# Optimization experiments

Measured on AMD Instinct MI355X. Metric: run time of the kernel, lower is better.

## Reference

```python
import jax, jax.numpy as jnp
import numpy as np

D_MODEL = 1024
NUM_HEADS = 16
D_K = D_MODEL // NUM_HEADS


def setup_inputs() -> dict:
    key = jax.random.key(0)
    kx, kq, kk, kv, ko = jax.random.split(key, 5)
    B, S = 4, 2048
    scale = 1.0 / np.sqrt(D_MODEL)
    return {
        "x": jax.random.normal(kx, (B, S, D_MODEL), dtype=jnp.float32),
        "W_q": jax.random.normal(kq, (D_MODEL, D_MODEL), dtype=jnp.float32) * scale,
        "W_k": jax.random.normal(kk, (D_MODEL, D_MODEL), dtype=jnp.float32) * scale,
        "W_v": jax.random.normal(kv, (D_MODEL, D_MODEL), dtype=jnp.float32) * scale,
        "W_o": jax.random.normal(ko, (D_MODEL, D_MODEL), dtype=jnp.float32) * scale,
    }


def reference(x, W_q, W_k, W_v, W_o):
    B, S, _ = x.shape
    # torch Linear: y = x @ W.T
    def proj(W):
        return (x @ W.T).reshape(B, S, NUM_HEADS, D_K).transpose(0, 2, 1, 3)  # [B,H,S,Dk]
    Q, K, V = proj(W_q), proj(W_k), proj(W_v)
    scores = jnp.einsum("bhqd,bhkd->bhqk", Q, K) / jnp.sqrt(jnp.float32(D_K))
    attn = jax.nn.softmax(scores, axis=-1)
    out = jnp.einsum("bhqk,bhkd->bhqd", attn, V)  # [B,H,S,Dk]
    out = out.transpose(0, 2, 1, 3).reshape(B, S, D_MODEL)
    return out @ W_o.T
```

## Files before the change

### kernel.cpp

```cpp
#include <hip/hip_runtime.h>
#include <hip/hip_bf16.h>

typedef unsigned short u16;
typedef __bf16 bf16x8 __attribute__((ext_vector_type(8)));
typedef float f32x4 __attribute__((ext_vector_type(4)));

#define DEV static __device__ __forceinline__

DEV u16 f2b(float f){
  union { float f; unsigned u; } v; v.f = f;
  unsigned r = (v.u + 0x7FFFu + ((v.u >> 16) & 1u)) >> 16;
  return (u16)r;
}

DEV unsigned pack2(float lo, float hi){
  __hip_bfloat162 h = __float22bfloat162_rn(float2{lo, hi});
  union { __hip_bfloat162 h; unsigned u; } c; c.h = h;
  return c.u;
}

DEV unsigned pack_trunc(float lo, float hi){
  union { float f; unsigned u; } a, b; a.f = lo; b.f = hi;
  return __builtin_amdgcn_perm(b.u, a.u, 0x07060302u);
}

DEV void gload16(const void* g, void* l){
  __builtin_amdgcn_global_load_lds((const __attribute__((address_space(1))) void*)g,
                                   (__attribute__((address_space(3))) void*)l, 16, 0, 0);
}

DEV f32x4 mfma16(bf16x8 a, bf16x8 b, f32x4 c){
  return __builtin_amdgcn_mfma_f32_16x16x32_bf16(a, b, c, 0, 0, 0);
}

__global__ void cvt_kernel(const float* __restrict__ src, u16* __restrict__ dst, int n4){
  int i = blockIdx.x * 256 + threadIdx.x;
  if (i < n4){
    float4 v = reinterpret_cast<const float4*>(src)[i];
    ushort4 o;
    o.x = f2b(v.x); o.y = f2b(v.y); o.z = f2b(v.z); o.w = f2b(v.w);
    reinterpret_cast<ushort4*>(dst)[i] = o;
  }
}

template<int MODE>
__global__ __launch_bounds__(256, 2)
void gemm_nt(const u16* __restrict__ A, const u16* __restrict__ B, void* __restrict__ Out, float scale){
  __shared__ __align__(16) u16 lsA[128*64];
  __shared__ __align__(16) u16 lsB[128*64];
  const int tid  = threadIdx.x;
  const int lane = tid & 63, wid = tid >> 6;
  const int g = lane >> 4, c15 = lane & 15;
  const int m0 = blockIdx.x * 128, n0 = blockIdx.y * 128;
  const int wm = (wid >> 1) * 64, wn = (wid & 1) * 64;
  const f32x4 vzero = {0.f, 0.f, 0.f, 0.f};

  f32x4 acc[4][4];
#pragma unroll
  for (int mi = 0; mi < 4; ++mi)
#pragma unroll
    for (int ni = 0; ni < 4; ++ni) acc[mi][ni] = vzero;

  for (int kt = 0; kt < 16; ++kt){
    __syncthreads();
#pragma unroll
    for (int i = 0; i < 4; ++i){
      int c = i * 256 + tid;
      int row = c >> 3, gc = (c & 7) ^ (row & 7);
      const u16* src;
      if constexpr (MODE == 2){
        int b = m0 >> 11, s = (m0 & 2047) + row;
        src = A + (((size_t)(b * 16 + kt) * 2048 + s) << 6) + (gc << 3);
      } else {
        src = A + ((size_t)(m0 + row) << 10) + (kt << 6) + (gc << 3);
      }
      gload16(src, lsA + (size_t)c * 8);
    }
#pragma unroll
    for (int i = 0; i < 4; ++i){
      int c = i * 256 + tid;
      int row = c >> 3, gc = (c & 7) ^ (row & 7);
      const u16* src = B + ((size_t)(n0 + row) << 10) + (kt << 6) + (gc << 3);
      gload16(src, lsB + (size_t)c * 8);
    }
    __syncthreads();

    bf16x8 af[4][2], bf[4][2];
#pragma unroll
    for (int mi = 0; mi < 4; ++mi)
#pragma unroll
      for (int kk = 0; kk < 2; ++kk){
        int ra = wm + mi * 16 + c15;
        af[mi][kk] = *reinterpret_cast<const bf16x8*>(lsA + ra * 64 + ((((kk << 2) + g) ^ (ra & 7)) << 3));
        int rb = wn + mi * 16 + c15;
        bf[mi][kk] = *reinterpret_cast<const bf16x8*>(lsB + rb * 64 + ((((kk << 2) + g) ^ (rb & 7)) << 3));
      }
#pragma unroll
    for (int mi = 0; mi < 4; ++mi)
#pragma unroll
      for (int ni = 0; ni < 4; ++ni){
        acc[mi][ni] = mfma16(af[mi][0], bf[ni][0], acc[mi][ni]);
        acc[mi][ni] = mfma16(af[mi][1], bf[ni][1], acc[mi][ni]);
      }
  }

#pragma unroll
  for (int mi = 0; mi < 4; ++mi)
#pragma unroll
    for (int ni = 0; ni < 4; ++ni){
      int mrow = m0 + wm + mi * 16 + g * 4;
      int ncol = n0 + wn + ni * 16 + c15;
      if constexpr (MODE == 0){
        int b = mrow >> 11, s = mrow & 2047;
        int h = ncol >> 6, dk = ncol & 63;
        u16* dst = (u16*)Out + (((size_t)(b * 16 + h) * 2048 + s) << 6) + dk;
#pragma unroll
        for (int r = 0; r < 4; ++r) dst[(size_t)r << 6] = f2b(acc[mi][ni][r] * scale);
      } else if constexpr (MODE == 1){
        int b = mrow >> 11, s = mrow & 2047;
        int h = ncol >> 6, dk = ncol & 63;
        ushort4 o;
        o.x = f2b(acc[mi][ni][0]); o.y = f2b(acc[mi][ni][1]);
        o.z = f2b(acc[mi][ni][2]); o.w = f2b(acc[mi][ni][3]);
        *reinterpret_cast<ushort4*>((u16*)Out + (((size_t)(b * 16 + h) * 64 + dk) << 11) + s) = o;
      } else {
        float* dst = (float*)Out + (size_t)mrow * 1024 + ncol;
#pragma unroll
        for (int r = 0; r < 4; ++r) dst[(size_t)r << 10] = acc[mi][ni][r];
      }
    }
}

__global__ __launch_bounds__(256, 4)
void attn_kernel(const u16* __restrict__ Q, const u16* __restrict__ K,
                 const u16* __restrict__ Vt, u16* __restrict__ O){
  __shared__ __align__(16) u16 lsK[64*64];
  __shared__ __align__(16) u16 lsV[64*64];
  __shared__ __align__(16) u16 lsP[4][32*64];
  const int tid  = threadIdx.x;
  const int lane = tid & 63, wid = tid >> 6;
  const int g = lane >> 4, c15 = lane & 15;
  const size_t hb = (size_t)blockIdx.y << 17;
  const int q0 = blockIdx.x * 128 + wid * 32;
  const f32x4 vzero = {0.f, 0.f, 0.f, 0.f};

#define STAGE_T(tt) do {                                                            \
    _Pragma("unroll")                                                               \
    for (int i_ = 0; i_ < 2; ++i_){                                                 \
      int c_ = i_ * 256 + tid;                                                      \
      int row_ = c_ >> 3, gc_ = (c_ & 7) ^ (row_ & 7);                              \
      gload16(K  + hb + ((size_t)((tt)*64 + row_) << 6) + (gc_ << 3), lsK + (size_t)c_ * 8); \
      gload16(Vt + hb + ((size_t)row_ << 11) + (tt)*64 + (gc_ << 3),  lsV + (size_t)c_ * 8); \
    }                                                                               \
  } while (0)

  bf16x8 qf[2][2];
#pragma unroll
  for (int mi = 0; mi < 2; ++mi)
#pragma unroll
    for (int kk = 0; kk < 2; ++kk)
      qf[mi][kk] = *reinterpret_cast<const bf16x8*>(Q + hb + ((size_t)(q0 + mi*16 + c15) << 6) + kk*32 + g*8);

  union { unsigned u[4]; bf16x8 v; } ou;
  ou.u[0] = ou.u[1] = ou.u[2] = ou.u[3] = 0x3F803F80u;
  const bf16x8 ones = ou.v;

  f32x4 oaccT[2][4];
  float mrun[2], lrun[2];
#pragma unroll
  for (int mi = 0; mi < 2; ++mi){
#pragma unroll
    for (int di = 0; di < 4; ++di) oaccT[mi][di] = vzero;
    mrun[mi] = -1e30f; lrun[mi] = 0.f;
  }

  char* pB = reinterpret_cast<char*>(lsP[wid]);

  for (int t = 0; t < 32; ++t){
    __syncthreads();
    STAGE_T(t);
    __syncthreads();

    bf16x8 kf[4][2];
#pragma unroll
    for (int ni = 0; ni < 4; ++ni)
#pragma unroll
      for (int kk = 0; kk < 2; ++kk){
        int row = ni*16 + c15;
        kf[ni][kk] = *reinterpret_cast<const bf16x8*>(lsK + row*64 + ((((kk<<2)+g) ^ (row&7)) << 3));
      }
    f32x4 sacc[2][4];
#pragma unroll
    for (int mi = 0; mi < 2; ++mi)
#pragma unroll
      for (int ni = 0; ni < 4; ++ni)
        sacc[mi][ni] = mfma16(kf[ni][1], qf[mi][1], mfma16(kf[ni][0], qf[mi][0], vzero));

#pragma unroll
    for (int mi = 0; mi < 2; ++mi){
      float a0 = fmaxf(fmaxf(sacc[mi][0][0], sacc[mi][0][1]), sacc[mi][0][2]);
      float a1 = fmaxf(fmaxf(sacc[mi][0][3], sacc[mi][1][0]), sacc[mi][1][1]);
      float a2 = fmaxf(fmaxf(sacc[mi][1][2], sacc[mi][1][3]), sacc[mi][2][0]);
      float a3 = fmaxf(fmaxf(sacc[mi][2][1], sacc[mi][2][2]), sacc[mi][2][3]);
      float a4 = fmaxf(fmaxf(sacc[mi][3][0], sacc[mi][3][1]), sacc[mi][3][2]);
      float b0 = fmaxf(fmaxf(a0, a1), a2);
      float b1 = fmaxf(fmaxf(a3, a4), sacc[mi][3][3]);
      float mt = fmaxf(b0, b1);
      mt = fmaxf(mt, __shfl_xor(mt, 16, 64));
      mt = fmaxf(mt, __shfl_xor(mt, 32, 64));
      if (mt > mrun[mi]){
        float f_ = __expf(mrun[mi] - mt);
        mrun[mi] = mt;
        lrun[mi] *= f_;
#pragma unroll
        for (int di = 0; di < 4; ++di) oaccT[mi][di] = oaccT[mi][di] * f_;
      }
      const float mn = mrun[mi];
      const int ql = mi*16 + c15;
#pragma unroll
      for (int ni = 0; ni < 4; ++ni){
        float p0 = __expf(sacc[mi][ni][0] - mn);
        float p1 = __expf(sacc[mi][ni][1] - mn);
        float p2 = __expf(sacc[mi][ni][2] - mn);
        float p3 = __expf(sacc[mi][ni][3] - mn);
        int off = ql*128 + ((((ni<<1)+(g>>1)) ^ (ql&7)) << 4) + ((g&1) << 3);
        *reinterpret_cast<uint2*>(pB + off) = make_uint2(pack_trunc(p0, p1), pack_trunc(p2, p3));
      }
    }

    bf16x8 vf[4][2];
#pragma unroll
    for (int di = 0; di < 4; ++di)
#pragma unroll
      for (int kk = 0; kk < 2; ++kk){
        int row = di*16 + c15;
        vf[di][kk] = *reinterpret_cast<const bf16x8*>(lsV + row*64 + ((((kk<<2)+g) ^ (row&7)) << 3));
      }

    asm volatile("s_waitcnt lgkmcnt(0)" ::: "memory");
    __builtin_amdgcn_sched_barrier(0);

    bf16x8 pf[2][2];
#pragma unroll
    for (int mi = 0; mi < 2; ++mi)
#pragma unroll
      for (int kk = 0; kk < 2; ++kk){
        int ql = mi*16 + c15;
        int off = ql*128 + ((((kk<<2)+g) ^ (ql&7)) << 4);
        pf[mi][kk] = *reinterpret_cast<const bf16x8*>(pB + off);
      }

#pragma unroll
    for (int mi = 0; mi < 2; ++mi){
      f32x4 ls = mfma16(ones, pf[mi][0], vzero);
      ls = mfma16(ones, pf[mi][1], ls);
      lrun[mi] += ls[0];
    }

#pragma unroll
    for (int mi = 0; mi < 2; ++mi)
#pragma unroll
      for (int di = 0; di < 4; ++di){
        oaccT[mi][di] = mfma16(vf[di][0], pf[mi][0], oaccT[mi][di]);
        oaccT[mi][di] = mfma16(vf[di][1], pf[mi][1], oaccT[mi][di]);
      }
  }

#pragma unroll
  for (int mi = 0; mi < 2; ++mi){
    float inv = 1.f / lrun[mi];
    int q = q0 + mi*16 + c15;
#pragma unroll
    for (int di = 0; di < 4; ++di){
      unsigned lo = pack2(oaccT[mi][di][0] * inv, oaccT[mi][di][1] * inv);
      unsigned hi = pack2(oaccT[mi][di][2] * inv, oaccT[mi][di][3] * inv);
      *reinterpret_cast<uint2*>(O + hb + ((size_t)q << 6) + di*16 + g*4) = make_uint2(lo, hi);
    }
  }
#undef STAGE_T
}

extern "C" void kernel_launch(void* const* d_in, const int* in_sizes, int n_in,
                              void* d_out, int out_size, void* d_ws, size_t ws_size,
                              hipStream_t stream){
  const float* x  = (const float*)d_in[0];
  const float* wq = (const float*)d_in[1];
  const float* wk = (const float*)d_in[2];
  const float* wv = (const float*)d_in[3];
  const float* wo = (const float*)d_in[4];
  float* out = (float*)d_out;
  char* ws = (char*)d_ws;
  u16* xb  = (u16*)(ws);
  u16* wqb = (u16*)(ws + (16u << 20));
  u16* wkb = (u16*)(ws + (18u << 20));
  u16* wvb = (u16*)(ws + (20u << 20));
  u16* wob = (u16*)(ws + (22u << 20));
  u16* Qb  = (u16*)(ws + (24u << 20));
  u16* Kb  = (u16*)(ws + (40u << 20));
  u16* Vtb = (u16*)(ws + (56u << 20));
  u16* Ob  = (u16*)(ws + (72u << 20));

  cvt_kernel<<<8192, 256, 0, stream>>>(x,  xb,  2097152);
  cvt_kernel<<<1024, 256, 0, stream>>>(wq, wqb, 262144);
  cvt_kernel<<<1024, 256, 0, stream>>>(wk, wkb, 262144);
  cvt_kernel<<<1024, 256, 0, stream>>>(wv, wvb, 262144);
  cvt_kernel<<<1024, 256, 0, stream>>>(wo, wob, 262144);

  dim3 gg(64, 8);
  gemm_nt<0><<<gg, 256, 0, stream>>>(xb, wqb, Qb, 0.125f);
  gemm_nt<0><<<gg, 256, 0, stream>>>(xb, wkb, Kb, 1.0f);
  gemm_nt<1><<<gg, 256, 0, stream>>>(xb, wvb, Vtb, 1.0f);
  attn_kernel<<<dim3(16, 64), 256, 0, stream>>>(Qb, Kb, Vtb, Ob);
  gemm_nt<2><<<gg, 256, 0, stream>>>(Ob, wob, out, 1.0f);
}
```

Measured before the change: 221.0 us.

## Double-buffer K/V tiles and pass P via lane shuffles instead of LDS

The attention loop now double-buffers the K and V LDS tiles, prefetching tile t+1 while computing tile t, which drops one of the two barriers per iteration. The probability tile P is no longer written to and read back from per-wave LDS. It is redistributed into MFMA operand layout with cross-lane shuffles. This is meant to overlap global loads with compute and cut LDS traffic, at the cost of twice the K/V LDS footprint, extra shuffle instructions, and reliance on the async load completing before the end-of-iteration barrier.

```diff
diff --git a/kernel.cpp b/kernel.cpp
--- a/kernel.cpp
+++ b/kernel.cpp
@@ -134,23 +134,26 @@
 __global__ __launch_bounds__(256, 4)
 void attn_kernel(const u16* __restrict__ Q, const u16* __restrict__ K,
                  const u16* __restrict__ Vt, u16* __restrict__ O){
-  __shared__ __align__(16) u16 lsK[64*64];
-  __shared__ __align__(16) u16 lsV[64*64];
-  __shared__ __align__(16) u16 lsP[4][32*64];
+  __shared__ __align__(16) u16 lsK[2][64*64];
+  __shared__ __align__(16) u16 lsV[2][64*64];
   const int tid  = threadIdx.x;
-  const int lane = tid & 63, wid = tid >> 6;
+  const int lane = tid & 63;
   const int g = lane >> 4, c15 = lane & 15;
   const size_t hb = (size_t)blockIdx.y << 17;
-  const int q0 = blockIdx.x * 128 + wid * 32;
+  const int q0 = blockIdx.x * 128 + (tid >> 6) * 32;
   const f32x4 vzero = {0.f, 0.f, 0.f, 0.f};
 
-#define STAGE_T(tt) do {                                                            \
+  const int srcA = c15 + ((lane & 16) << 1);
+  const int srcB = srcA + 16;
+  const bool hihalf = (lane >= 32);
+
+#define STAGE_T(tb, tt) do {                                                        \
     _Pragma("unroll")                                                               \
     for (int i_ = 0; i_ < 2; ++i_){                                                 \
       int c_ = i_ * 256 + tid;                                                      \
       int row_ = c_ >> 3, gc_ = (c_ & 7) ^ (row_ & 7);                              \
-      gload16(K  + hb + ((size_t)((tt)*64 + row_) << 6) + (gc_ << 3), lsK + (size_t)c_ * 8); \
-      gload16(Vt + hb + ((size_t)row_ << 11) + (tt)*64 + (gc_ << 3),  lsV + (size_t)c_ * 8); \
+      gload16(K  + hb + ((size_t)((tt)*64 + row_) << 6) + (gc_ << 3), lsK[tb] + (size_t)c_ * 8); \
+      gload16(Vt + hb + ((size_t)row_ << 11) + (tt)*64 + (gc_ << 3),  lsV[tb] + (size_t)c_ * 8); \
     }                                                                               \
   } while (0)
 
@@ -174,12 +177,14 @@
     mrun[mi] = -1e30f; lrun[mi] = 0.f;
   }
 
-  char* pB = reinterpret_cast<char*>(lsP[wid]);
+  STAGE_T(0, 0);
+  __syncthreads();
 
   for (int t = 0; t < 32; ++t){
-    __syncthreads();
-    STAGE_T(t);
-    __syncthreads();
+    const int cur = t & 1;
+    if (t < 31) STAGE_T(cur ^ 1, t + 1);
+    const u16* bK = lsK[cur];
+    const u16* bV = lsV[cur];
 
     bf16x8 kf[4][2];
 #pragma unroll
@@ -187,7 +192,7 @@
 #pragma unroll
       for (int kk = 0; kk < 2; ++kk){
         int row = ni*16 + c15;
-        kf[ni][kk] = *reinterpret_cast<const bf16x8*>(lsK + row*64 + ((((kk<<2)+g) ^ (row&7)) << 3));
+        kf[ni][kk] = *reinterpret_cast<const bf16x8*>(bK + row*64 + ((((kk<<2)+g) ^ (row&7)) << 3));
       }
     f32x4 sacc[2][4];
 #pragma unroll
@@ -196,6 +201,7 @@
       for (int ni = 0; ni < 4; ++ni)
         sacc[mi][ni] = mfma16(kf[ni][1], qf[mi][1], mfma16(kf[ni][0], qf[mi][0], vzero));
 
+    unsigned pk[2][4][2];
 #pragma unroll
     for (int mi = 0; mi < 2; ++mi){
       float a0 = fmaxf(fmaxf(sacc[mi][0][0], sacc[mi][0][1]), sacc[mi][0][2]);
@@ -216,17 +222,33 @@
         for (int di = 0; di < 4; ++di) oaccT[mi][di] = oaccT[mi][di] * f_;
       }
       const float mn = mrun[mi];
-      const int ql = mi*16 + c15;
 #pragma unroll
       for (int ni = 0; ni < 4; ++ni){
         float p0 = __expf(sacc[mi][ni][0] - mn);
         float p1 = __expf(sacc[mi][ni][1] - mn);
         float p2 = __expf(sacc[mi][ni][2] - mn);
         float p3 = __expf(sacc[mi][ni][3] - mn);
-        int off = ql*128 + ((((ni<<1)+(g>>1)) ^ (ql&7)) << 4) + ((g&1) << 3);
-        *reinterpret_cast<uint2*>(pB + off) = make_uint2(pack_trunc(p0, p1), pack_trunc(p2, p3));
-      }
-    }
+        pk[mi][ni][0] = pack_trunc(p0, p1);
+        pk[mi][ni][1] = pack_trunc(p2, p3);
+      }
+    }
+
+    bf16x8 pf[2][2];
+#pragma unroll
+    for (int mi = 0; mi < 2; ++mi)
+#pragma unroll
+      for (int kk = 0; kk < 2; ++kk){
+        union { unsigned u[4]; bf16x8 v; } pu;
+#pragma unroll
+        for (int w = 0; w < 4; ++w){
+          const int p = w & 1;
+          const int src = (w < 2) ? srcA : srcB;
+          unsigned va = (unsigned)__shfl((int)pk[mi][2*kk    ][p], src, 64);
+          unsigned vb = (unsigned)__shfl((int)pk[mi][2*kk + 1][p], src, 64);
+          pu.u[w] = hihalf ? vb : va;
+        }
+        pf[mi][kk] = pu.v;
+      }
 
     bf16x8 vf[4][2];
 #pragma unroll
@@ -234,20 +256,7 @@
 #pragma unroll
       for (int kk = 0; kk < 2; ++kk){
         int row = di*16 + c15;
-        vf[di][kk] = *reinterpret_cast<const bf16x8*>(lsV + row*64 + ((((kk<<2)+g) ^ (row&7)) << 3));
-      }
-
-    asm volatile("s_waitcnt lgkmcnt(0)" ::: "memory");
-    __builtin_amdgcn_sched_barrier(0);
-
-    bf16x8 pf[2][2];
-#pragma unroll
-    for (int mi = 0; mi < 2; ++mi)
-#pragma unroll
-      for (int kk = 0; kk < 2; ++kk){
-        int ql = mi*16 + c15;
-        int off = ql*128 + ((((kk<<2)+g) ^ (ql&7)) << 4);
-        pf[mi][kk] = *reinterpret_cast<const bf16x8*>(pB + off);
+        vf[di][kk] = *reinterpret_cast<const bf16x8*>(bV + row*64 + ((((kk<<2)+g) ^ (row&7)) << 3));
       }
 
 #pragma unroll
@@ -264,6 +273,8 @@
         oaccT[mi][di] = mfma16(vf[di][0], pf[mi][0], oaccT[mi][di]);
         oaccT[mi][di] = mfma16(vf[di][1], pf[mi][1], oaccT[mi][di]);
       }
+
+    __syncthreads();
   }
 
 #pragma unroll
```

After: 222.5 us. Within noise of the previous version (+0.7%).
